# Kernel tuning notes

Hardware: AMD Instinct MI355X
Metric: run time of the kernel (lower is better)

The kernel has to match this reference:

```python
import jax, jax.numpy as jnp
import numpy as np

GAMMA = 0.1
EPS = 1e-10


def setup_inputs() -> dict:
    key = jax.random.key(0)
    ks = jax.random.split(key, 7)
    B, N, D = 1024, 2048, 128
    return {
        "target_embed": jax.random.normal(ks[0], (B, D), dtype=jnp.float32),
        "candidate_embeds": jax.random.normal(ks[1], (B, N, D), dtype=jnp.float32),
        "Wq": jax.random.normal(ks[2], (D, D), dtype=jnp.float32) * 0.05,
        "bq": jax.random.normal(ks[3], (D,), dtype=jnp.float32) * 0.05,
        "Wk": jax.random.normal(ks[4], (D, D), dtype=jnp.float32) * 0.05,
        "bk": jax.random.normal(ks[5], (D,), dtype=jnp.float32) * 0.05,
        "u": jax.random.uniform(ks[6], (B, N), dtype=jnp.float32),
        "num_neighbors": 32,
    }


def reference(target_embed, candidate_embeds, Wq, bq, Wk, bk, u, num_neighbors):
    B, N, D = candidate_embeds.shape
    scale = jnp.sqrt(jnp.float32(D))
    # Linear projections (torch Linear: x @ W.T + b)
    Q = target_embed @ Wq.T + bq                      # [B, D]
    K = jnp.einsum('bnd,ed->bne', candidate_embeds, Wk) + bk  # [B, N, D]
    scores = jnp.einsum('bd,bnd->bn', Q, K) / scale   # [B, N]
    p = jax.nn.softmax(scores, axis=-1)
    p = (1.0 - GAMMA) * p + GAMMA / N                 # mix with uniform
    # multinomial without replacement == Gumbel top-k on log-probs
    gumbel = -jnp.log(-jnp.log(u + EPS) + EPS)        # [B, N]
    _, sampled_idx = jax.lax.top_k(jnp.log(p) + gumbel, num_neighbors)  # [B, k]
    return sampled_idx
```

## Files before the change

kernel.cpp:

```cpp
#include <hip/hip_runtime.h>
#include <cmath>
#include <cfloat>
#include <climits>

constexpr int D    = 128;
constexpr int NT   = 512;
constexpr int NW   = NT / 64;
constexpr int KMAX = 64;
constexpr float EPS_ = 1e-10f;

template <int CTRL>
__device__ __forceinline__ float dpp_add(float x) {
  int y = __builtin_amdgcn_update_dpp(0, __float_as_int(x), CTRL, 0xf, 0xf, false);
  return x + __int_as_float(y);
}
template <int CTRL>
__device__ __forceinline__ float dpp_max(float x) {
  int y = __builtin_amdgcn_update_dpp(__float_as_int(x), __float_as_int(x),
                                      CTRL, 0xf, 0xf, false);
  return fmaxf(x, __int_as_float(y));
}
__device__ __forceinline__ float dpp_sum32(float x) {
  x = dpp_add<0x111>(x);
  x = dpp_add<0x112>(x);
  x = dpp_add<0x114>(x);
  x = dpp_add<0x118>(x);
  x = dpp_add<0x142>(x);
  return x;
}
__device__ __forceinline__ float dpp_sum64(float x) {
  x = dpp_sum32(x);
  x = dpp_add<0x143>(x);
  return __int_as_float(__builtin_amdgcn_readlane(__float_as_int(x), 63));
}
__device__ __forceinline__ float dpp_max64(float x) {
  x = dpp_max<0x111>(x);
  x = dpp_max<0x112>(x);
  x = dpp_max<0x114>(x);
  x = dpp_max<0x118>(x);
  x = dpp_max<0x142>(x);
  x = dpp_max<0x143>(x);
  return __int_as_float(__builtin_amdgcn_readlane(__float_as_int(x), 63));
}

__global__ __launch_bounds__(NT, 8) void fused2_kernel(
    const float* __restrict__ target, const float* __restrict__ cand,
    const float* __restrict__ Wq, const float* __restrict__ bq,
    const float* __restrict__ Wk, const float* __restrict__ u,
    const int* __restrict__ kptr, int* __restrict__ out, int N)
{
  extern __shared__ __align__(16) float sS[];
  __shared__ __align__(16) float sTgt[D];
  __shared__ __align__(16) float sQ[D];
  __shared__ __align__(16) float sQt[D];
  __shared__ float redM[NW];
  __shared__ float cV[NW * KMAX];
  __shared__ int   cI[NW * KMAX];

  const int b    = blockIdx.x;
  const int tid  = threadIdx.x;
  const int lane = tid & 63;
  const int wave = tid >> 6;

  if (tid < D) sTgt[tid] = target[(size_t)b * D + tid];
  __syncthreads();
  if (tid < D) {
    float acc = 0.f;
    const float* wrow = Wq + (size_t)tid * D;
    #pragma unroll 8
    for (int e = 0; e < D; ++e) acc += sTgt[e] * wrow[e];
    sQ[tid] = acc + bq[tid];
  }
  __syncthreads();
  if (tid < D) {
    float acc = 0.f;
    #pragma unroll 8
    for (int d = 0; d < D; ++d) acc += sQ[d] * Wk[(size_t)d * D + tid];
    sQt[tid] = acc;
  }
  __syncthreads();

  const int p    = lane & 31;
  const int half = lane >> 5;
  const float4 qf = ((const float4*)sQt)[p];
  const float inv_scale = 1.0f / sqrtf((float)D);
  const float* base = cand + (size_t)b * N * D;
  const bool writer = (p == 31);

  for (int n0 = wave * 8; n0 < N; n0 += NW * 8) {
    const float4* r0 = (const float4*)(base + (size_t)(n0 + 0) * D) + lane;
    const float4* r1 = (const float4*)(base + (size_t)(n0 + 2) * D) + lane;
    const float4* r2 = (const float4*)(base + (size_t)(n0 + 4) * D) + lane;
    const float4* r3 = (const float4*)(base + (size_t)(n0 + 6) * D) + lane;
    float4 a0 = *r0, a1 = *r1, a2 = *r2, a3 = *r3;
    float s0 = a0.x * qf.x + a0.y * qf.y + a0.z * qf.z + a0.w * qf.w;
    float s1 = a1.x * qf.x + a1.y * qf.y + a1.z * qf.z + a1.w * qf.w;
    float s2 = a2.x * qf.x + a2.y * qf.y + a2.z * qf.z + a2.w * qf.w;
    float s3 = a3.x * qf.x + a3.y * qf.y + a3.z * qf.z + a3.w * qf.w;
    s0 = dpp_sum32(s0);
    s1 = dpp_sum32(s1);
    s2 = dpp_sum32(s2);
    s3 = dpp_sum32(s3);
    if (writer) {
      sS[n0 + 0 + half] = s0 * inv_scale;
      sS[n0 + 2 + half] = s1 * inv_scale;
      sS[n0 + 4 + half] = s2 * inv_scale;
      sS[n0 + 6 + half] = s3 * inv_scale;
    }
  }
  __syncthreads();

  const int iv = wave * 256 + lane * 4;
  float4 sv = *(const float4*)(sS + iv);
  float v0 = sv.x, v1 = sv.y, v2 = sv.z, v3 = sv.w;

  float m = fmaxf(fmaxf(v0, v1), fmaxf(v2, v3));
  m = dpp_max64(m);
  if (lane == 0) redM[wave] = m;
  __syncthreads();
  m = redM[0];
  #pragma unroll
  for (int w = 1; w < NW; ++w) m = fmaxf(m, redM[w]);
  __syncthreads();

  float ssum = expf(v0 - m) + expf(v1 - m) + expf(v2 - m) + expf(v3 - m);
  ssum = dpp_sum64(ssum);
  if (lane == 0) redM[wave] = ssum;
  __syncthreads();
  float Z = redM[0];
  #pragma unroll
  for (int w = 1; w < NW; ++w) Z += redM[w];
  __syncthreads();

  const float mixc = (float)(0.1 / (double)N);
  float4 uv = *(const float4*)(u + (size_t)b * N + iv);
  v0 = logf(0.9f * (expf(v0 - m) / Z) + mixc) + (-logf(-logf(uv.x + EPS_) + EPS_));
  v1 = logf(0.9f * (expf(v1 - m) / Z) + mixc) + (-logf(-logf(uv.y + EPS_) + EPS_));
  v2 = logf(0.9f * (expf(v2 - m) / Z) + mixc) + (-logf(-logf(uv.z + EPS_) + EPS_));
  v3 = logf(0.9f * (expf(v3 - m) / Z) + mixc) + (-logf(-logf(uv.w + EPS_) + EPS_));

  const int k = kptr[0];

  for (int i = 0; i < k; ++i) {
    float bv = v0; int bj = 0;
    if (v1 > bv) { bv = v1; bj = 1; }
    if (v2 > bv) { bv = v2; bj = 2; }
    if (v3 > bv) { bv = v3; bj = 3; }
    int bidx = iv + bj;
    for (int s = 32; s; s >>= 1) {
      float ov = __shfl_xor(bv, s);
      int   oi = __shfl_xor(bidx, s);
      if (ov > bv || (ov == bv && oi < bidx)) { bv = ov; bidx = oi; }
    }
    if (lane == ((bidx & 255) >> 2)) {
      int off = bidx & 3;
      if (off == 0) v0 = -FLT_MAX;
      if (off == 1) v1 = -FLT_MAX;
      if (off == 2) v2 = -FLT_MAX;
      if (off == 3) v3 = -FLT_MAX;
    }
    if (lane == 0) { cV[wave * KMAX + i] = bv; cI[wave * KMAX + i] = bidx; }
  }
  __syncthreads();

  if (wave == 0) {
    const int tot = NW * k;
    float mv[8]; int mi[8];
    #pragma unroll
    for (int t = 0; t < 8; ++t) {
      int c = lane + 64 * t;
      if (c < tot) {
        int w = c / k, i = c % k;
        mv[t] = cV[w * KMAX + i]; mi[t] = cI[w * KMAX + i];
      } else { mv[t] = -FLT_MAX; mi[t] = INT_MAX; }
    }
    for (int i = 0; i < k; ++i) {
      float bv = mv[0]; int bidx = mi[0];
      #pragma unroll
      for (int t = 1; t < 8; ++t)
        if (mv[t] > bv || (mv[t] == bv && mi[t] < bidx)) { bv = mv[t]; bidx = mi[t]; }
      for (int s = 32; s; s >>= 1) {
        float ov = __shfl_xor(bv, s);
        int   oi = __shfl_xor(bidx, s);
        if (ov > bv || (ov == bv && oi < bidx)) { bv = ov; bidx = oi; }
      }
      #pragma unroll
      for (int t = 0; t < 8; ++t) if (mi[t] == bidx) mv[t] = -FLT_MAX;
      if (lane == 0) out[(size_t)b * k + i] = bidx;
    }
  }
}

constexpr int NTF = 512;
constexpr int NWF = NTF / 64;
__global__ __launch_bounds__(NTF, 8) void fused_kernel(
    const float* __restrict__ target, const float* __restrict__ cand,
    const float* __restrict__ Wq, const float* __restrict__ bq,
    const float* __restrict__ Wk, const float* __restrict__ u,
    const int* __restrict__ kptr, int* __restrict__ out, int N)
{
  extern __shared__ float sS[];
  __shared__ float sTgt[D];
  __shared__ float sQ[D];
  __shared__ float sQt[D];
  __shared__ float redV[NWF];
  __shared__ int   redI[NWF];

  const int b = blockIdx.x, tid = threadIdx.x;
  const int lane = tid & 63, wave = tid >> 6;

  if (tid < D) sTgt[tid] = target[(size_t)b * D + tid];
  __syncthreads();
  if (tid < D) {
    float acc = 0.f;
    const float* wrow = Wq + (size_t)tid * D;
    #pragma unroll 8
    for (int e = 0; e < D; ++e) acc += sTgt[e] * wrow[e];
    sQ[tid] = acc + bq[tid];
  }
  __syncthreads();
  if (tid < D) {
    float acc = 0.f;
    #pragma unroll 8
    for (int d = 0; d < D; ++d) acc += sQ[d] * Wk[(size_t)d * D + tid];
    sQt[tid] = acc;
  }
  __syncthreads();

  const int grp = lane >> 4, gl = lane & 15;
  float q0 = sQt[gl*8+0], q1 = sQt[gl*8+1], q2 = sQt[gl*8+2], q3 = sQt[gl*8+3];
  float q4 = sQt[gl*8+4], q5 = sQt[gl*8+5], q6 = sQt[gl*8+6], q7 = sQt[gl*8+7];
  const float scale = sqrtf((float)D);
  const int rstride = NWF * 4;
  int n = wave * 4 + grp;
  for (; n + rstride < N; n += 2 * rstride) {
    const float4* r0 = (const float4*)(cand + ((size_t)b * N + n) * D);
    const float4* r1 = (const float4*)(cand + ((size_t)b * N + n + rstride) * D);
    float4 a0 = r0[gl*2+0], a1 = r0[gl*2+1], c0 = r1[gl*2+0], c1 = r1[gl*2+1];
    float p0 = a0.x*q0 + a0.y*q1 + a0.z*q2 + a0.w*q3 + a1.x*q4 + a1.y*q5 + a1.z*q6 + a1.w*q7;
    float p1 = c0.x*q0 + c0.y*q1 + c0.z*q2 + c0.w*q3 + c1.x*q4 + c1.y*q5 + c1.z*q6 + c1.w*q7;
    p0 += __shfl_xor(p0,1); p1 += __shfl_xor(p1,1);
    p0 += __shfl_xor(p0,2); p1 += __shfl_xor(p1,2);
    p0 += __shfl_xor(p0,4); p1 += __shfl_xor(p1,4);
    p0 += __shfl_xor(p0,8); p1 += __shfl_xor(p1,8);
    if (gl == 0) { sS[n] = p0 / scale; sS[n + rstride] = p1 / scale; }
  }
  if (n < N) {
    const float4* r0 = (const float4*)(cand + ((size_t)b * N + n) * D);
    float4 a0 = r0[gl*2+0], a1 = r0[gl*2+1];
    float p0 = a0.x*q0 + a0.y*q1 + a0.z*q2 + a0.w*q3 + a1.x*q4 + a1.y*q5 + a1.z*q6 + a1.w*q7;
    p0 += __shfl_xor(p0,1); p0 += __shfl_xor(p0,2); p0 += __shfl_xor(p0,4); p0 += __shfl_xor(p0,8);
    if (gl == 0) sS[n] = p0 / scale;
  }
  __syncthreads();

  float m = -FLT_MAX;
  for (int i = tid; i < N; i += NTF) m = fmaxf(m, sS[i]);
  for (int s = 32; s; s >>= 1) m = fmaxf(m, __shfl_xor(m, s));
  if (lane == 0) redV[wave] = m;
  __syncthreads();
  m = redV[0];
  #pragma unroll
  for (int w = 1; w < NWF; ++w) m = fmaxf(m, redV[w]);
  __syncthreads();

  float ssum = 0.f;
  for (int i = tid; i < N; i += NTF) ssum += expf(sS[i] - m);
  for (int s = 32; s; s >>= 1) ssum += __shfl_xor(ssum, s);
  if (lane == 0) redV[wave] = ssum;
  __syncthreads();
  float Z = redV[0];
  #pragma unroll
  for (int w = 1; w < NWF; ++w) Z += redV[w];
  __syncthreads();

  const float mixc = (float)(0.1 / (double)N);
  for (int i = tid; i < N; i += NTF) {
    float pmix = 0.9f * (expf(sS[i] - m) / Z) + mixc;
    float uvs = u[(size_t)b * N + i];
    float g = -logf(-logf(uvs + EPS_) + EPS_);
    sS[i] = logf(pmix) + g;
  }
  __syncthreads();

  const int k = kptr[0];
  for (int i = 0; i < k; ++i) {
    float bv = -FLT_MAX; int bi = N;
    for (int j = tid; j < N; j += NTF) {
      float vv = sS[j];
      if (vv > bv || (vv == bv && j < bi)) { bv = vv; bi = j; }
    }
    for (int s = 32; s; s >>= 1) {
      float ov = __shfl_xor(bv, s); int oi = __shfl_xor(bi, s);
      if (ov > bv || (ov == bv && oi < bi)) { bv = ov; bi = oi; }
    }
    if (lane == 0) { redV[wave] = bv; redI[wave] = bi; }
    __syncthreads();
    if (tid == 0) {
      float fv = redV[0]; int fi = redI[0];
      #pragma unroll
      for (int w = 1; w < NWF; ++w)
        if (redV[w] > fv || (redV[w] == fv && redI[w] < fi)) { fv = redV[w]; fi = redI[w]; }
      out[(size_t)b * k + i] = fi;
      sS[fi] = -FLT_MAX;
    }
    __syncthreads();
  }
}

extern "C" void kernel_launch(void* const* d_in, const int* in_sizes, int n_in,
                              void* d_out, int out_size, void* d_ws, size_t ws_size,
                              hipStream_t stream) {
  const float* target = (const float*)d_in[0];
  const float* cand   = (const float*)d_in[1];
  const float* Wq     = (const float*)d_in[2];
  const float* bq     = (const float*)d_in[3];
  const float* Wk     = (const float*)d_in[4];
  const float* bk     = (const float*)d_in[5];
  const float* u      = (const float*)d_in[6];
  const int*   kptr   = (const int*)d_in[7];
  (void)bk; (void)n_in; (void)d_ws; (void)ws_size;

  const int B = in_sizes[0] / D;
  const int N = in_sizes[1] / (B * D);
  const int k = out_size / B;

  if (N == NT * 4 && (N % 64) == 0 && k <= KMAX) {
    fused2_kernel<<<B, NT, N * sizeof(float), stream>>>(
        target, cand, Wq, bq, Wk, u, kptr, (int*)d_out, N);
  } else {
    fused_kernel<<<B, NTF, N * sizeof(float), stream>>>(
        target, cand, Wq, bq, Wk, u, kptr, (int*)d_out, N);
  }
}
```

Before: 245.9 us.

## Double-buffer candidate loads with nontemporal hints and per-block slot rotation

```diff
diff --git a/kernel.cpp b/kernel.cpp
--- a/kernel.cpp
+++ b/kernel.cpp
@@ -8,6 +8,12 @@
 constexpr int NW   = NT / 64;
 constexpr int KMAX = 64;
 constexpr float EPS_ = 1e-10f;
+
+typedef float vf4 __attribute__((ext_vector_type(4)));
+__device__ __forceinline__ float4 ntload(const float4* p) {
+  vf4 v = __builtin_nontemporal_load((const vf4*)p);
+  return make_float4(v.x, v.y, v.z, v.w);
+}
 
 template <int CTRL>
 __device__ __forceinline__ float dpp_add(float x) {
@@ -43,7 +49,7 @@
   return __int_as_float(__builtin_amdgcn_readlane(__float_as_int(x), 63));
 }
 
-__global__ __launch_bounds__(NT, 8) void fused2_kernel(
+__global__ __launch_bounds__(NT, 6) void fused2_kernel(
     const float* __restrict__ target, const float* __restrict__ cand,
     const float* __restrict__ Wq, const float* __restrict__ bq,
     const float* __restrict__ Wk, const float* __restrict__ u,
@@ -84,29 +90,58 @@
   const int half = lane >> 5;
   const float4 qf = ((const float4*)sQt)[p];
   const float inv_scale = 1.0f / sqrtf((float)D);
-  const float* base = cand + (size_t)b * N * D;
+  const float4* cb4 = (const float4*)(cand + (size_t)b * N * D);
   const bool writer = (p == 31);
 
-  for (int n0 = wave * 8; n0 < N; n0 += NW * 8) {
-    const float4* r0 = (const float4*)(base + (size_t)(n0 + 0) * D) + lane;
-    const float4* r1 = (const float4*)(base + (size_t)(n0 + 2) * D) + lane;
-    const float4* r2 = (const float4*)(base + (size_t)(n0 + 4) * D) + lane;
-    const float4* r3 = (const float4*)(base + (size_t)(n0 + 6) * D) + lane;
-    float4 a0 = *r0, a1 = *r1, a2 = *r2, a3 = *r3;
-    float s0 = a0.x * qf.x + a0.y * qf.y + a0.z * qf.z + a0.w * qf.w;
-    float s1 = a1.x * qf.x + a1.y * qf.y + a1.z * qf.z + a1.w * qf.w;
-    float s2 = a2.x * qf.x + a2.y * qf.y + a2.z * qf.z + a2.w * qf.w;
-    float s3 = a3.x * qf.x + a3.y * qf.y + a3.z * qf.z + a3.w * qf.w;
-    s0 = dpp_sum32(s0);
-    s1 = dpp_sum32(s1);
-    s2 = dpp_sum32(s2);
-    s3 = dpp_sum32(s3);
-    if (writer) {
-      sS[n0 + 0 + half] = s0 * inv_scale;
-      sS[n0 + 2 + half] = s1 * inv_scale;
-      sS[n0 + 4 + half] = s2 * inv_scale;
-      sS[n0 + 6 + half] = s3 * inv_scale;
-    }
+  const int SLOTS = N / 8;
+  const int ITERS = SLOTS / NW;
+  const int rot   = (b * 97) & (SLOTS - 1);
+
+  int slotA = (wave + rot) & (SLOTS - 1);
+  const float4* pA = cb4 + (size_t)slotA * 256 + lane;
+  float4 A0 = ntload(pA), A1 = ntload(pA + 64), A2 = ntload(pA + 128), A3 = ntload(pA + 192);
+
+  for (int i = 0; i < ITERS; i += 2) {
+    const int slotB = (wave + NW * (i + 1) + rot) & (SLOTS - 1);
+    const float4* pB = cb4 + (size_t)slotB * 256 + lane;
+    float4 B0 = ntload(pB), B1 = ntload(pB + 64), B2 = ntload(pB + 128), B3 = ntload(pB + 192);
+
+    {
+      float s0 = A0.x * qf.x + A0.y * qf.y + A0.z * qf.z + A0.w * qf.w;
+      float s1 = A1.x * qf.x + A1.y * qf.y + A1.z * qf.z + A1.w * qf.w;
+      float s2 = A2.x * qf.x + A2.y * qf.y + A2.z * qf.z + A2.w * qf.w;
+      float s3 = A3.x * qf.x + A3.y * qf.y + A3.z * qf.z + A3.w * qf.w;
+      s0 = dpp_sum32(s0); s1 = dpp_sum32(s1); s2 = dpp_sum32(s2); s3 = dpp_sum32(s3);
+      const int n0 = slotA * 8;
+      if (writer) {
+        sS[n0 + 0 + half] = s0 * inv_scale;
+        sS[n0 + 2 + half] = s1 * inv_scale;
+        sS[n0 + 4 + half] = s2 * inv_scale;
+        sS[n0 + 6 + half] = s3 * inv_scale;
+      }
+    }
+
+    const int slotA2 = (wave + NW * (i + 2) + rot) & (SLOTS - 1);
+    if (i + 2 < ITERS) {
+      const float4* pA2 = cb4 + (size_t)slotA2 * 256 + lane;
+      A0 = ntload(pA2); A1 = ntload(pA2 + 64); A2 = ntload(pA2 + 128); A3 = ntload(pA2 + 192);
+    }
+
+    {
+      float s0 = B0.x * qf.x + B0.y * qf.y + B0.z * qf.z + B0.w * qf.w;
+      float s1 = B1.x * qf.x + B1.y * qf.y + B1.z * qf.z + B1.w * qf.w;
+      float s2 = B2.x * qf.x + B2.y * qf.y + B2.z * qf.z + B2.w * qf.w;
+      float s3 = B3.x * qf.x + B3.y * qf.y + B3.z * qf.z + B3.w * qf.w;
+      s0 = dpp_sum32(s0); s1 = dpp_sum32(s1); s2 = dpp_sum32(s2); s3 = dpp_sum32(s3);
+      const int n0 = slotB * 8;
+      if (writer) {
+        sS[n0 + 0 + half] = s0 * inv_scale;
+        sS[n0 + 2 + half] = s1 * inv_scale;
+        sS[n0 + 4 + half] = s2 * inv_scale;
+        sS[n0 + 6 + half] = s3 * inv_scale;
+      }
+    }
+    slotA = slotA2;
   }
   __syncthreads();
 
```

Result: faster. 226.7 us (-7.8%).
